# Kernel optimization log

Hardware: AMD Instinct MI355X
Metric: run time of the kernel (lower is better)

The kernel has to match this reference:

```python
import jax, jax.numpy as jnp
import numpy as np

NUM_HEADS = 12


def setup_inputs() -> dict:
    key = jax.random.key(0)
    ks = jax.random.split(key, 9)
    B, T, C = 4, 2048, 768
    s = 1.0 / np.sqrt(C)
    return {
        "x": jax.random.normal(ks[0], (B, T, C), dtype=jnp.float32),
        "wq": jax.random.normal(ks[1], (C, C), dtype=jnp.float32) * s,
        "bq": jnp.zeros((C,), dtype=jnp.float32),
        "wk": jax.random.normal(ks[2], (C, C), dtype=jnp.float32) * s,
        "bk": jnp.zeros((C,), dtype=jnp.float32),
        "wv": jax.random.normal(ks[3], (C, C), dtype=jnp.float32) * s,
        "bv": jnp.zeros((C,), dtype=jnp.float32),
        "wo": jax.random.normal(ks[4], (C, C), dtype=jnp.float32) * s,
        "bo": jnp.zeros((C,), dtype=jnp.float32),
    }


def reference(x, wq, bq, wk, bk, wv, bv, wo, bo):
    B, T, C = x.shape
    H = NUM_HEADS
    D = C // H
    scale = D ** -0.5
    # projections: weights stored as [in, out] so y = x @ w + b
    q = (x @ wq + bq).reshape(B, T, H, D).transpose(0, 2, 1, 3)  # [B,H,T,D]
    k = (x @ wk + bk).reshape(B, T, H, D).transpose(0, 2, 1, 3)
    v = (x @ wv + bv).reshape(B, T, H, D).transpose(0, 2, 1, 3)
    scores = jnp.einsum("bhqd,bhkd->bhqk", q, k) * scale  # [B,H,T,T]
    probs = jax.nn.softmax(scores, axis=-1)
    out = jnp.einsum("bhqk,bhkd->bhqd", probs, v)  # [B,H,T,D]
    out = out.transpose(0, 2, 1, 3).reshape(B, T, C)
    return out @ wo + bo
```

## Files before the change

kernel.cpp:

```cpp
#include <hip/hip_runtime.h>
#include <math.h>

#define NB 4
#define T_SEQ 2048
#define C_DIM 768
#define NH 12
#define HD 64
#define M_TOK (NB * T_SEQ)
#define NE ((size_t)M_TOK * C_DIM)
#define WE ((size_t)C_DIM * C_DIM)
#define QSCALE 0.18033688011112042f

typedef short bf16x8 __attribute__((ext_vector_type(8)));
typedef float f32x4 __attribute__((ext_vector_type(4)));
typedef unsigned short u16x4 __attribute__((ext_vector_type(4)));
typedef unsigned short u16x8 __attribute__((ext_vector_type(8)));
typedef unsigned short ushort_t;

__device__ __forceinline__ unsigned short f2bf(float x) {
    unsigned u = __float_as_uint(x);
    u += 0x7FFFu + ((u >> 16) & 1u);
    return (unsigned short)(u >> 16);
}
__device__ __forceinline__ float bf2f(unsigned short h) {
    return __uint_as_float(((unsigned)h) << 16);
}
__device__ __forceinline__ int sw128(int row, int bytecol) {
    return row * 128 + (bytecol ^ ((row & 7) << 4));
}
__device__ __forceinline__ void gload16(const ushort_t* gp, ushort_t* lp) {
    __builtin_amdgcn_global_load_lds(
        (const __attribute__((address_space(1))) unsigned int*)(const void*)gp,
        (__attribute__((address_space(3))) unsigned int*)(void*)lp, 16, 0, 0);
}

__global__ __launch_bounds__(256) void prep(
    const float* __restrict__ X,
    const float* __restrict__ wq, const float* __restrict__ wk,
    const float* __restrict__ wv, const float* __restrict__ wo,
    ushort_t* __restrict__ XH, ushort_t* __restrict__ Wbase)
{
    __shared__ float T[64][65];
    const int tid = threadIdx.x;
    const int bid = blockIdx.x;

    if (bid < 3072) {
        const size_t i = ((size_t)bid * 256 + tid) * 8;
        const float4 f0 = *(const float4*)&X[i];
        const float4 f1 = *(const float4*)&X[i + 4];
        const float xs[8] = {f0.x, f0.y, f0.z, f0.w, f1.x, f1.y, f1.z, f1.w};
        u16x8 h;
        #pragma unroll
        for (int j = 0; j < 8; ++j) h[j] = f2bf(xs[j]);
        *(u16x8*)&XH[i] = h;
        return;
    }

    const int r_ = bid - 3072;
    const int z = r_ / 144;
    const int rem = r_ % 144;
    const int ti = rem / 12, nj = rem % 12;
    const float* W = (z == 0) ? wq : (z == 1) ? wk : (z == 2) ? wv : wo;
    ushort_t* TH = Wbase + (size_t)z * 2 * WE;
    ushort_t* TL = TH + WE;
    {
        const int r = tid >> 2, cq = (tid & 3) * 16;
        #pragma unroll
        for (int j = 0; j < 4; ++j) {
            const float4 f = *(const float4*)&W[(size_t)(ti * 64 + r) * C_DIM + nj * 64 + cq + j * 4];
            T[r][cq + j * 4 + 0] = f.x;
            T[r][cq + j * 4 + 1] = f.y;
            T[r][cq + j * 4 + 2] = f.z;
            T[r][cq + j * 4 + 3] = f.w;
        }
    }
    __syncthreads();
    {
        const int n = tid >> 2, kq = (tid & 3) * 16;
        u16x8 h0, h1, l0, l1;
        #pragma unroll
        for (int j = 0; j < 8; ++j) {
            float v = T[kq + j][n];
            unsigned short hh = f2bf(v);
            h0[j] = hh; l0[j] = f2bf(v - bf2f(hh));
            v = T[kq + 8 + j][n];
            hh = f2bf(v);
            h1[j] = hh; l1[j] = f2bf(v - bf2f(hh));
        }
        const size_t o = (size_t)(nj * 64 + n) * C_DIM + ti * 64 + kq;
        *(u16x8*)&TH[o] = h0; *(u16x8*)&TH[o + 8] = h1;
        *(u16x8*)&TL[o] = l0; *(u16x8*)&TL[o + 8] = l1;
    }
}

__global__ __launch_bounds__(256, 4) void gemm_qkv(
    const ushort_t* __restrict__ XH,
    const ushort_t* __restrict__ WQH, const ushort_t* __restrict__ WKH,
    const ushort_t* __restrict__ WVH,
    const float* __restrict__ bq, const float* __restrict__ bk,
    const float* __restrict__ bv,
    ushort_t* __restrict__ Qo, ushort_t* __restrict__ Ko, ushort_t* __restrict__ VTo)
{
    __shared__ ushort_t TA[2][128 * 32];
    __shared__ ushort_t TB[2][128 * 32];

    const int tid = threadIdx.x, lane = tid & 63, w = tid >> 6;
    const int l15 = lane & 15, g = lane >> 4;
    const int wr = w >> 1, wc = w & 1;

    int bid = (int)blockIdx.x;
    bid = (bid & 7) * 144 + (bid >> 3);
    const int bm = bid / 18, bn = bid % 18;
    const int wsel = bn / 6, bnw = bn % 6;

    const ushort_t* BH = (wsel == 0) ? WQH : (wsel == 1) ? WKH : WVH;
    const float* bias = (wsel == 0) ? bq : (wsel == 1) ? bk : bv;

    f32x4 acc[4][4];
    #pragma unroll
    for (int m = 0; m < 4; ++m)
        #pragma unroll
        for (int n = 0; n < 4; ++n) acc[m][n] = (f32x4){0.f, 0.f, 0.f, 0.f};

    auto stage = [&](int buf, int k0) {
        #pragma unroll
        for (int p = 0; p < 4; ++p) {
            const int cb = 256 * p + 64 * w;
            const int c  = cb + lane;
            const int row = (c & 511) >> 2;
            const int slot = (c & 3) ^ ((row >> 1) & 3);
            if (cb < 512)
                gload16(XH + ((size_t)bm * 128 + row) * C_DIM + k0 + slot * 8,
                        &TA[buf][(cb & 511) * 8]);
            else
                gload16(BH + ((size_t)bnw * 128 + row) * C_DIM + k0 + slot * 8,
                        &TB[buf][(cb & 511) * 8]);
        }
    };

    stage(0, 0);
    int cur = 0;
    if (wsel < 2) {
        for (int k0 = 0; k0 < C_DIM; k0 += 32) {
            __syncthreads();
            if (k0 + 32 < C_DIM) stage(cur ^ 1, k0 + 32);
            bf16x8 ah[4], bh_[4];
            #pragma unroll
            for (int m = 0; m < 4; ++m) {
                const int r = 64 * wr + 16 * m + l15;
                const int off = r * 64 + ((g ^ ((r >> 1) & 3)) << 4);
                ah[m] = *(const bf16x8*)((const char*)TA[cur] + off);
            }
            #pragma unroll
            for (int n = 0; n < 4; ++n) {
                const int r = 64 * wc + 16 * n + l15;
                const int off = r * 64 + ((g ^ ((r >> 1) & 3)) << 4);
                bh_[n] = *(const bf16x8*)((const char*)TB[cur] + off);
            }
            #pragma unroll
            for (int m = 0; m < 4; ++m)
                #pragma unroll
                for (int n = 0; n < 4; ++n)
                    acc[m][n] = __builtin_amdgcn_mfma_f32_16x16x32_bf16(bh_[n], ah[m], acc[m][n], 0, 0, 0);
            cur ^= 1;
        }
        const float oscale = (wsel == 0) ? QSCALE : 1.0f;
        ushort_t* OH = (wsel == 0) ? Qo : Ko;
        #pragma unroll
        for (int n = 0; n < 4; ++n) {
            const int colw0 = bnw * 128 + 64 * wc + 16 * n + 4 * g;
            const float4 bv4 = *(const float4*)&bias[colw0];
            const float bvr[4] = {bv4.x, bv4.y, bv4.z, bv4.w};
            const int h = colw0 >> 6, d0 = colw0 & 63;
            #pragma unroll
            for (int m = 0; m < 4; ++m) {
                const int t = bm * 128 + 64 * wr + 16 * m + l15;
                const int b = t >> 11, tt = t & (T_SEQ - 1);
                u16x4 ph;
                #pragma unroll
                for (int r = 0; r < 4; ++r)
                    ph[r] = f2bf((acc[m][n][r] + bvr[r]) * oscale);
                *(u16x4*)&OH[(((size_t)b * NH + h) * T_SEQ + tt) * HD + d0] = ph;
            }
        }
    } else {
        for (int k0 = 0; k0 < C_DIM; k0 += 32) {
            __syncthreads();
            if (k0 + 32 < C_DIM) stage(cur ^ 1, k0 + 32);
            bf16x8 ah[4], bh_[4];
            #pragma unroll
            for (int m = 0; m < 4; ++m) {
                const int r = 64 * wr + 16 * m + l15;
                const int off = r * 64 + ((g ^ ((r >> 1) & 3)) << 4);
                ah[m] = *(const bf16x8*)((const char*)TA[cur] + off);
            }
            #pragma unroll
            for (int n = 0; n < 4; ++n) {
                const int r = 64 * wc + 16 * n + l15;
                const int off = r * 64 + ((g ^ ((r >> 1) & 3)) << 4);
                bh_[n] = *(const bf16x8*)((const char*)TB[cur] + off);
            }
            #pragma unroll
            for (int m = 0; m < 4; ++m)
                #pragma unroll
                for (int n = 0; n < 4; ++n)
                    acc[m][n] = __builtin_amdgcn_mfma_f32_16x16x32_bf16(ah[m], bh_[n], acc[m][n], 0, 0, 0);
            cur ^= 1;
        }
        #pragma unroll
        for (int n = 0; n < 4; ++n) {
            const int colw = bnw * 128 + 64 * wc + 16 * n + l15;
            const float bv_ = bias[colw];
            const int h = colw >> 6, d = colw & 63;
            #pragma unroll
            for (int m = 0; m < 4; ++m) {
                const int row0 = bm * 128 + 64 * wr + 16 * m + 4 * g;
                u16x4 ph;
                #pragma unroll
                for (int r = 0; r < 4; ++r) ph[r] = f2bf(acc[m][n][r] + bv_);
                const int b = row0 >> 11, t0 = row0 & (T_SEQ - 1);
                *(u16x4*)&VTo[(((size_t)b * NH + h) * HD + d) * T_SEQ + t0] = ph;
            }
        }
    }
}

__global__ __launch_bounds__(256, 4) void gemm_out(
    const ushort_t* __restrict__ AB,
    const ushort_t* __restrict__ BH, const ushort_t* __restrict__ BL,
    const float* __restrict__ bias, float* __restrict__ OutF)
{
    __shared__ ushort_t TA[2][128 * 32];
    __shared__ ushort_t TB[2][2][64 * 32];

    const int tid = threadIdx.x, lane = tid & 63, w = tid >> 6;
    const int l15 = lane & 15, g = lane >> 4;
    const int wr = w >> 1, wc = w & 1;

    int bid = (int)blockIdx.x;
    bid = (bid & 7) * 96 + (bid >> 3);
    const int bm = bid / 12, bn = bid % 12;

    f32x4 acc[4][2];
    #pragma unroll
    for (int m = 0; m < 4; ++m)
        #pragma unroll
        for (int n = 0; n < 2; ++n) acc[m][n] = (f32x4){0.f, 0.f, 0.f, 0.f};

    auto stage = [&](int buf, int k0) {
        #pragma unroll
        for (int p = 0; p < 4; ++p) {
            const int c = w + 4 * p;
            if (c < 8) {
                const int row = c * 16 + (lane >> 2);
                const int slot = (lane & 3) ^ ((row >> 1) & 3);
                gload16(AB + ((size_t)bm * 128 + row) * C_DIM + k0 + slot * 8,
                        &TA[buf][c * 512]);
            } else {
                const int t_ = (c - 8) >> 2;
                const int cc = c & 3;
                const int row = cc * 16 + (lane >> 2);
                const int slot = (lane & 3) ^ ((row >> 1) & 3);
                const ushort_t* src = (t_ ? BL : BH) + ((size_t)bn * 64 + row) * C_DIM + k0 + slot * 8;
                gload16(src, &TB[buf][t_][cc * 512]);
            }
        }
    };

    stage(0, 0);
    int cur = 0;
    for (int k0 = 0; k0 < C_DIM; k0 += 32) {
        __syncthreads();
        if (k0 + 32 < C_DIM) stage(cur ^ 1, k0 + 32);

        bf16x8 a_[4], bh_[2], bl_[2];
        #pragma unroll
        for (int m = 0; m < 4; ++m) {
            const int r = 64 * wr + 16 * m + l15;
            const int off = r * 64 + ((g ^ ((r >> 1) & 3)) << 4);
            a_[m] = *(const bf16x8*)((const char*)TA[cur] + off);
        }
        #pragma unroll
        for (int n = 0; n < 2; ++n) {
            const int r = 32 * wc + 16 * n + l15;
            const int off = r * 64 + ((g ^ ((r >> 1) & 3)) << 4);
            bh_[n] = *(const bf16x8*)((const char*)TB[cur][0] + off);
            bl_[n] = *(const bf16x8*)((const char*)TB[cur][1] + off);
        }
        #pragma unroll
        for (int m = 0; m < 4; ++m)
            #pragma unroll
            for (int n = 0; n < 2; ++n) {
                acc[m][n] = __builtin_amdgcn_mfma_f32_16x16x32_bf16(a_[m], bh_[n], acc[m][n], 0, 0, 0);
                acc[m][n] = __builtin_amdgcn_mfma_f32_16x16x32_bf16(a_[m], bl_[n], acc[m][n], 0, 0, 0);
            }
        cur ^= 1;
    }

    #pragma unroll
    for (int n = 0; n < 2; ++n) {
        const int col = bn * 64 + 32 * wc + 16 * n + l15;
        const float bv = bias[col];
        #pragma unroll
        for (int m = 0; m < 4; ++m) {
            const int row0 = bm * 128 + 64 * wr + 16 * m + 4 * g;
            #pragma unroll
            for (int r = 0; r < 4; ++r)
                OutF[(size_t)(row0 + r) * C_DIM + col] = acc[m][n][r] + bv;
        }
    }
}

__global__ __launch_bounds__(256, 3) void attn_fuse9(
    const ushort_t* __restrict__ QB, const ushort_t* __restrict__ KB,
    const ushort_t* __restrict__ VTB, ushort_t* __restrict__ ABo)
{
    __shared__ ushort_t Ks[2][64 * 64];
    __shared__ ushort_t Vt[2][64 * 64];
    __shared__ ushort_t Pm[4][32 * 64];

    const int tid = threadIdx.x, lane = tid & 63, w = tid >> 6;
    const int l15 = lane & 15, g = lane >> 4;

    int bid = (int)blockIdx.x;
    bid = (bid & 7) * 96 + (bid >> 3);
    const int bh = bid >> 4, qt = bid & 15;
    const int b = bh / NH, h = bh % NH;

    bf16x8 qf0[2], qf1[2];
    #pragma unroll
    for (int kc = 0; kc < 2; ++kc) {
        const size_t base = ((size_t)bh * T_SEQ + qt * 128 + 32 * w + l15) * HD + kc * 32 + g * 8;
        qf0[kc] = *(const bf16x8*)&QB[base];
        qf1[kc] = *(const bf16x8*)&QB[base + (size_t)16 * HD];
    }

    bf16x8 onesf;
    #pragma unroll
    for (int j = 0; j < 8; ++j) onesf[j] = (short)0x3F80;

    f32x4 o0[4], o1[4];
    #pragma unroll
    for (int nd = 0; nd < 4; ++nd) {
        o0[nd] = (f32x4){0.f, 0.f, 0.f, 0.f};
        o1[nd] = (f32x4){0.f, 0.f, 0.f, 0.f};
    }
    f32x4 ol0 = (f32x4){0.f, 0.f, 0.f, 0.f};
    f32x4 ol1 = (f32x4){0.f, 0.f, 0.f, 0.f};

    const ushort_t* kb = KB + (size_t)bh * T_SEQ * HD;
    const ushort_t* vb = VTB + (size_t)bh * HD * T_SEQ;
    const int swz = (l15 & 7) << 4;

    const ushort_t *gK0, *gK1, *gV0, *gV1;
    {
        const int c0 = w * 64 + lane;
        const int r0 = c0 >> 3;
        const int cb0 = ((c0 & 7) * 16) ^ ((r0 & 7) << 4);
        gK0 = kb + (size_t)r0 * HD + (cb0 >> 1);
        gV0 = vb + (size_t)r0 * T_SEQ + (cb0 >> 1);
        const int c1 = c0 + 256;
        const int r1 = c1 >> 3;
        const int cb1 = ((c1 & 7) * 16) ^ ((r1 & 7) << 4);
        gK1 = kb + (size_t)r1 * HD + (cb1 >> 1);
        gV1 = vb + (size_t)r1 * T_SEQ + (cb1 >> 1);
    }
    ushort_t* dK0 = &Ks[0][w * 512];
    ushort_t* dK1 = &Ks[0][2048 + w * 512];
    ushort_t* dV0 = &Vt[0][w * 512];
    ushort_t* dV1 = &Vt[0][2048 + w * 512];

    for (int kt = 0; kt < T_SEQ; kt += 128) {
        __syncthreads();
        gload16(gK0, dK0);
        gload16(gK1, dK1);
        gload16(gV0, dV0);
        gload16(gV1, dV1);
        gload16(gK0 + (size_t)64 * HD, dK0 + 4096);
        gload16(gK1 + (size_t)64 * HD, dK1 + 4096);
        gload16(gV0 + 64, dV0 + 4096);
        gload16(gV1 + 64, dV1 + 4096);
        gK0 += (size_t)128 * HD; gK1 += (size_t)128 * HD;
        gV0 += 128; gV1 += 128;
        __syncthreads();

        #pragma unroll
        for (int half = 0; half < 2; ++half) {
            const char* ksb = (const char*)Ks[half];
            const char* vtb = (const char*)Vt[half];

            f32x4 s0[4], s1[4];
            #pragma unroll
            for (int nb = 0; nb < 4; ++nb) {
                s0[nb] = (f32x4){0.f, 0.f, 0.f, 0.f};
                s1[nb] = (f32x4){0.f, 0.f, 0.f, 0.f};
            }
            __builtin_amdgcn_s_setprio(1);
            #pragma unroll
            for (int kc = 0; kc < 2; ++kc)
                #pragma unroll
                for (int nb = 0; nb < 4; ++nb) {
                    const bf16x8 kf = *(const bf16x8*)(ksb + sw128(16 * nb + l15, kc * 64 + g * 16));
                    s0[nb] = __builtin_amdgcn_mfma_f32_16x16x32_bf16(kf, qf0[kc], s0[nb], 0, 0, 0);
                    s1[nb] = __builtin_amdgcn_mfma_f32_16x16x32_bf16(kf, qf1[kc], s1[nb], 0, 0, 0);
                }
            __builtin_amdgcn_s_setprio(0);

            #pragma unroll
            for (int nb = 0; nb < 4; ++nb) {
                const float a0 = __builtin_amdgcn_exp2f(s0[nb][0]);
                const float a1 = __builtin_amdgcn_exp2f(s0[nb][1]);
                const float a2 = __builtin_amdgcn_exp2f(s0[nb][2]);
                const float a3 = __builtin_amdgcn_exp2f(s0[nb][3]);
                const unsigned dwa0 = __builtin_amdgcn_perm(
                    __float_as_uint(a1), __float_as_uint(a0), 0x07060302u);
                const unsigned dwa1 = __builtin_amdgcn_perm(
                    __float_as_uint(a3), __float_as_uint(a2), 0x07060302u);
                *(uint2*)((char*)Pm[w] + l15 * 128 + ((32 * nb + 8 * g) ^ swz)) =
                    make_uint2(dwa0, dwa1);

                const float b0 = __builtin_amdgcn_exp2f(s1[nb][0]);
                const float b1 = __builtin_amdgcn_exp2f(s1[nb][1]);
                const float b2 = __builtin_amdgcn_exp2f(s1[nb][2]);
                const float b3 = __builtin_amdgcn_exp2f(s1[nb][3]);
                const unsigned dwb0 = __builtin_amdgcn_perm(
                    __float_as_uint(b1), __float_as_uint(b0), 0x07060302u);
                const unsigned dwb1 = __builtin_amdgcn_perm(
                    __float_as_uint(b3), __float_as_uint(b2), 0x07060302u);
                *(uint2*)((char*)Pm[w] + (16 + l15) * 128 + ((32 * nb + 8 * g) ^ swz)) =
                    make_uint2(dwb0, dwb1);
            }

            __builtin_amdgcn_s_setprio(1);
            #pragma unroll
            for (int kc2 = 0; kc2 < 2; ++kc2) {
                const bf16x8 pb0 = *(const bf16x8*)((const char*)Pm[w] + l15 * 128 + ((kc2 * 64 + g * 16) ^ swz));
                const bf16x8 pb1 = *(const bf16x8*)((const char*)Pm[w] + (16 + l15) * 128 + ((kc2 * 64 + g * 16) ^ swz));
                #pragma unroll
                for (int nd = 0; nd < 4; ++nd) {
                    const bf16x8 vf = *(const bf16x8*)(vtb + sw128(16 * nd + l15, kc2 * 64 + g * 16));
                    o0[nd] = __builtin_amdgcn_mfma_f32_16x16x32_bf16(vf, pb0, o0[nd], 0, 0, 0);
                    o1[nd] = __builtin_amdgcn_mfma_f32_16x16x32_bf16(vf, pb1, o1[nd], 0, 0, 0);
                }
                ol0 = __builtin_amdgcn_mfma_f32_16x16x32_bf16(onesf, pb0, ol0, 0, 0, 0);
                ol1 = __builtin_amdgcn_mfma_f32_16x16x32_bf16(onesf, pb1, ol1, 0, 0, 0);
            }
            __builtin_amdgcn_s_setprio(0);
        }
    }

    const float inv0 = 1.0f / ol0[0];
    const float inv1 = 1.0f / ol1[0];
    const int t0 = qt * 128 + 32 * w + l15;
    #pragma unroll
    for (int nd = 0; nd < 4; ++nd) {
        u16x4 h0_, h1_;
        #pragma unroll
        for (int r = 0; r < 4; ++r) {
            h0_[r] = f2bf(o0[nd][r] * inv0);
            h1_[r] = f2bf(o1[nd][r] * inv1);
        }
        const size_t col = h * HD + 16 * nd + 4 * g;
        *(u16x4*)&ABo[((size_t)b * T_SEQ + t0) * C_DIM + col] = h0_;
        *(u16x4*)&ABo[((size_t)b * T_SEQ + t0 + 16) * C_DIM + col] = h1_;
    }
}

extern "C" void kernel_launch(void* const* d_in, const int* in_sizes, int n_in,
                              void* d_out, int out_size, void* d_ws, size_t ws_size,
                              hipStream_t stream)
{
    const float* x  = (const float*)d_in[0];
    const float* wq = (const float*)d_in[1];
    const float* bq = (const float*)d_in[2];
    const float* wk = (const float*)d_in[3];
    const float* bk = (const float*)d_in[4];
    const float* wv = (const float*)d_in[5];
    const float* bv = (const float*)d_in[6];
    const float* wo = (const float*)d_in[7];
    const float* bo = (const float*)d_in[8];

    ushort_t* Wbase = (ushort_t*)d_ws;
    ushort_t* WQ_H = Wbase;
    ushort_t* WK_H = Wbase + 2 * WE;
    ushort_t* WV_H = Wbase + 4 * WE;
    ushort_t* WO_H = Wbase + 6 * WE;
    ushort_t* WO_L = WO_H + WE;
    ushort_t* X_H  = Wbase + 8 * WE;
    ushort_t* K_B  = X_H + 2 * NE;
    ushort_t* VT_B = K_B + NE;
    ushort_t* Q_B = (ushort_t*)d_out;
    ushort_t* A_B = X_H;

    const dim3 blk(256);

    prep<<<3648, blk, 0, stream>>>(x, wq, wk, wv, wo, X_H, Wbase);

    gemm_qkv<<<1152, blk, 0, stream>>>(X_H, WQ_H, WK_H, WV_H,
                                       bq, bk, bv, Q_B, K_B, VT_B);

    attn_fuse9<<<768, blk, 0, stream>>>(Q_B, K_B, VT_B, A_B);

    gemm_out<<<768, blk, 0, stream>>>(A_B, WO_H, WO_L, bo, (float*)d_out);
}
```

Measured before the change: 147.2 us.

## Switch attention to 32x32x16 MFMA and keep P in registers via permlane swap

Rewrites the attention kernel to use 32x32x16 bf16 MFMA tiles instead of 16x16x32. The exponentiated score accumulator is repacked directly into the B-operand layout with permlane32_swap, so the per-wave LDS staging buffer for P and its stores and loads go away. The prep kernel also writes the low-part weight split only for the output projection weight, skipping unused stores for Q/K/V. This raises accumulator register pressure (three f32x16 accumulators plus the score tiles), which may affect occupancy at the three-blocks-per-SM bound.

```diff
diff --git a/kernel.cpp b/kernel.cpp
--- a/kernel.cpp
+++ b/kernel.cpp
@@ -13,6 +13,8 @@
 
 typedef short bf16x8 __attribute__((ext_vector_type(8)));
 typedef float f32x4 __attribute__((ext_vector_type(4)));
+typedef float f32x16 __attribute__((ext_vector_type(16)));
+typedef unsigned u32x2 __attribute__((ext_vector_type(2)));
 typedef unsigned short u16x4 __attribute__((ext_vector_type(4)));
 typedef unsigned short u16x8 __attribute__((ext_vector_type(8)));
 typedef unsigned short ushort_t;
@@ -32,6 +34,9 @@
     __builtin_amdgcn_global_load_lds(
         (const __attribute__((address_space(1))) unsigned int*)(const void*)gp,
         (__attribute__((address_space(3))) unsigned int*)(void*)lp, 16, 0, 0);
+}
+__device__ __forceinline__ unsigned pkbf(float hi, float lo) {
+    return __builtin_amdgcn_perm(__float_as_uint(hi), __float_as_uint(lo), 0x07060302u);
 }
 
 __global__ __launch_bounds__(256) void prep(
@@ -89,7 +94,9 @@
         }
         const size_t o = (size_t)(nj * 64 + n) * C_DIM + ti * 64 + kq;
         *(u16x8*)&TH[o] = h0; *(u16x8*)&TH[o + 8] = h1;
-        *(u16x8*)&TL[o] = l0; *(u16x8*)&TL[o + 8] = l1;
+        if (z == 3) {
+            *(u16x8*)&TL[o] = l0; *(u16x8*)&TL[o + 8] = l1;
+        }
     }
 }
 
@@ -311,46 +318,35 @@
     }
 }
 
-__global__ __launch_bounds__(256, 3) void attn_fuse9(
+__global__ __launch_bounds__(256, 3) void attn_fuse11(
     const ushort_t* __restrict__ QB, const ushort_t* __restrict__ KB,
     const ushort_t* __restrict__ VTB, ushort_t* __restrict__ ABo)
 {
     __shared__ ushort_t Ks[2][64 * 64];
     __shared__ ushort_t Vt[2][64 * 64];
-    __shared__ ushort_t Pm[4][32 * 64];
 
     const int tid = threadIdx.x, lane = tid & 63, w = tid >> 6;
-    const int l15 = lane & 15, g = lane >> 4;
+    const int l31 = lane & 31, hl = lane >> 5;
 
     int bid = (int)blockIdx.x;
     bid = (bid & 7) * 96 + (bid >> 3);
     const int bh = bid >> 4, qt = bid & 15;
-    const int b = bh / NH, h = bh % NH;
-
-    bf16x8 qf0[2], qf1[2];
-    #pragma unroll
-    for (int kc = 0; kc < 2; ++kc) {
-        const size_t base = ((size_t)bh * T_SEQ + qt * 128 + 32 * w + l15) * HD + kc * 32 + g * 8;
-        qf0[kc] = *(const bf16x8*)&QB[base];
-        qf1[kc] = *(const bf16x8*)&QB[base + (size_t)16 * HD];
-    }
+    const int b = bh / NH, hed = bh % NH;
+
+    bf16x8 qf[4];
+    const size_t qrow = (size_t)bh * T_SEQ + qt * 128 + 32 * w + l31;
+    #pragma unroll
+    for (int ks = 0; ks < 4; ++ks)
+        qf[ks] = *(const bf16x8*)&QB[qrow * HD + ks * 16 + 8 * hl];
 
     bf16x8 onesf;
     #pragma unroll
     for (int j = 0; j < 8; ++j) onesf[j] = (short)0x3F80;
 
-    f32x4 o0[4], o1[4];
-    #pragma unroll
-    for (int nd = 0; nd < 4; ++nd) {
-        o0[nd] = (f32x4){0.f, 0.f, 0.f, 0.f};
-        o1[nd] = (f32x4){0.f, 0.f, 0.f, 0.f};
-    }
-    f32x4 ol0 = (f32x4){0.f, 0.f, 0.f, 0.f};
-    f32x4 ol1 = (f32x4){0.f, 0.f, 0.f, 0.f};
+    f32x16 oA = (f32x16)(0.f), oB = (f32x16)(0.f), ol = (f32x16)(0.f);
 
     const ushort_t* kb = KB + (size_t)bh * T_SEQ * HD;
     const ushort_t* vb = VTB + (size_t)bh * HD * T_SEQ;
-    const int swz = (l15 & 7) << 4;
 
     const ushort_t *gK0, *gK1, *gV0, *gV1;
     {
@@ -369,6 +365,22 @@
     ushort_t* dK1 = &Ks[0][2048 + w * 512];
     ushort_t* dV0 = &Vt[0][w * 512];
     ushort_t* dV1 = &Vt[0][2048 + w * 512];
+
+    auto mkfrag = [&](const f32x16& s, int base) -> bf16x8 {
+        const unsigned D0 = pkbf(__builtin_amdgcn_exp2f(s[base + 1]),
+                                 __builtin_amdgcn_exp2f(s[base + 0]));
+        const unsigned D1 = pkbf(__builtin_amdgcn_exp2f(s[base + 3]),
+                                 __builtin_amdgcn_exp2f(s[base + 2]));
+        const unsigned D2 = pkbf(__builtin_amdgcn_exp2f(s[base + 5]),
+                                 __builtin_amdgcn_exp2f(s[base + 4]));
+        const unsigned D3 = pkbf(__builtin_amdgcn_exp2f(s[base + 7]),
+                                 __builtin_amdgcn_exp2f(s[base + 6]));
+        const u32x2 r02 = __builtin_amdgcn_permlane32_swap(D0, D2, false, false);
+        const u32x2 r13 = __builtin_amdgcn_permlane32_swap(D1, D3, false, false);
+        union { unsigned u[4]; bf16x8 v; } cv;
+        cv.u[0] = r02[0]; cv.u[1] = r13[0]; cv.u[2] = r02[1]; cv.u[3] = r13[1];
+        return cv.v;
+    };
 
     for (int kt = 0; kt < T_SEQ; kt += 128) {
         __syncthreads();
@@ -389,80 +401,52 @@
             const char* ksb = (const char*)Ks[half];
             const char* vtb = (const char*)Vt[half];
 
-            f32x4 s0[4], s1[4];
-            #pragma unroll
-            for (int nb = 0; nb < 4; ++nb) {
-                s0[nb] = (f32x4){0.f, 0.f, 0.f, 0.f};
-                s1[nb] = (f32x4){0.f, 0.f, 0.f, 0.f};
-            }
+            f32x16 sA = (f32x16)(0.f), sB = (f32x16)(0.f);
             __builtin_amdgcn_s_setprio(1);
             #pragma unroll
-            for (int kc = 0; kc < 2; ++kc)
-                #pragma unroll
-                for (int nb = 0; nb < 4; ++nb) {
-                    const bf16x8 kf = *(const bf16x8*)(ksb + sw128(16 * nb + l15, kc * 64 + g * 16));
-                    s0[nb] = __builtin_amdgcn_mfma_f32_16x16x32_bf16(kf, qf0[kc], s0[nb], 0, 0, 0);
-                    s1[nb] = __builtin_amdgcn_mfma_f32_16x16x32_bf16(kf, qf1[kc], s1[nb], 0, 0, 0);
-                }
+            for (int ks = 0; ks < 4; ++ks) {
+                const int bc = ks * 32 + 16 * hl;
+                const bf16x8 kfA = *(const bf16x8*)(ksb + sw128(l31, bc));
+                const bf16x8 kfB = *(const bf16x8*)(ksb + sw128(32 + l31, bc));
+                sA = __builtin_amdgcn_mfma_f32_32x32x16_bf16(kfA, qf[ks], sA, 0, 0, 0);
+                sB = __builtin_amdgcn_mfma_f32_32x32x16_bf16(kfB, qf[ks], sB, 0, 0, 0);
+            }
             __builtin_amdgcn_s_setprio(0);
 
-            #pragma unroll
-            for (int nb = 0; nb < 4; ++nb) {
-                const float a0 = __builtin_amdgcn_exp2f(s0[nb][0]);
-                const float a1 = __builtin_amdgcn_exp2f(s0[nb][1]);
-                const float a2 = __builtin_amdgcn_exp2f(s0[nb][2]);
-                const float a3 = __builtin_amdgcn_exp2f(s0[nb][3]);
-                const unsigned dwa0 = __builtin_amdgcn_perm(
-                    __float_as_uint(a1), __float_as_uint(a0), 0x07060302u);
-                const unsigned dwa1 = __builtin_amdgcn_perm(
-                    __float_as_uint(a3), __float_as_uint(a2), 0x07060302u);
-                *(uint2*)((char*)Pm[w] + l15 * 128 + ((32 * nb + 8 * g) ^ swz)) =
-                    make_uint2(dwa0, dwa1);
-
-                const float b0 = __builtin_amdgcn_exp2f(s1[nb][0]);
-                const float b1 = __builtin_amdgcn_exp2f(s1[nb][1]);
-                const float b2 = __builtin_amdgcn_exp2f(s1[nb][2]);
-                const float b3 = __builtin_amdgcn_exp2f(s1[nb][3]);
-                const unsigned dwb0 = __builtin_amdgcn_perm(
-                    __float_as_uint(b1), __float_as_uint(b0), 0x07060302u);
-                const unsigned dwb1 = __builtin_amdgcn_perm(
-                    __float_as_uint(b3), __float_as_uint(b2), 0x07060302u);
-                *(uint2*)((char*)Pm[w] + (16 + l15) * 128 + ((32 * nb + 8 * g) ^ swz)) =
-                    make_uint2(dwb0, dwb1);
-            }
+            bf16x8 pb0 = mkfrag(sA, 0);
+            bf16x8 pb1 = mkfrag(sA, 8);
+            bf16x8 pb2 = mkfrag(sB, 0);
+            bf16x8 pb3 = mkfrag(sB, 8);
 
             __builtin_amdgcn_s_setprio(1);
             #pragma unroll
-            for (int kc2 = 0; kc2 < 2; ++kc2) {
-                const bf16x8 pb0 = *(const bf16x8*)((const char*)Pm[w] + l15 * 128 + ((kc2 * 64 + g * 16) ^ swz));
-                const bf16x8 pb1 = *(const bf16x8*)((const char*)Pm[w] + (16 + l15) * 128 + ((kc2 * 64 + g * 16) ^ swz));
-                #pragma unroll
-                for (int nd = 0; nd < 4; ++nd) {
-                    const bf16x8 vf = *(const bf16x8*)(vtb + sw128(16 * nd + l15, kc2 * 64 + g * 16));
-                    o0[nd] = __builtin_amdgcn_mfma_f32_16x16x32_bf16(vf, pb0, o0[nd], 0, 0, 0);
-                    o1[nd] = __builtin_amdgcn_mfma_f32_16x16x32_bf16(vf, pb1, o1[nd], 0, 0, 0);
-                }
-                ol0 = __builtin_amdgcn_mfma_f32_16x16x32_bf16(onesf, pb0, ol0, 0, 0, 0);
-                ol1 = __builtin_amdgcn_mfma_f32_16x16x32_bf16(onesf, pb1, ol1, 0, 0, 0);
+            for (int ki = 0; ki < 4; ++ki) {
+                const bf16x8 pb = (ki == 0) ? pb0 : (ki == 1) ? pb1 : (ki == 2) ? pb2 : pb3;
+                const int bc = ki * 32 + 16 * hl;
+                const bf16x8 vfA = *(const bf16x8*)(vtb + sw128(l31, bc));
+                const bf16x8 vfB = *(const bf16x8*)(vtb + sw128(32 + l31, bc));
+                oA = __builtin_amdgcn_mfma_f32_32x32x16_bf16(vfA, pb, oA, 0, 0, 0);
+                oB = __builtin_amdgcn_mfma_f32_32x32x16_bf16(vfB, pb, oB, 0, 0, 0);
+                ol = __builtin_amdgcn_mfma_f32_32x32x16_bf16(onesf, pb, ol, 0, 0, 0);
             }
             __builtin_amdgcn_s_setprio(0);
         }
     }
 
-    const float inv0 = 1.0f / ol0[0];
-    const float inv1 = 1.0f / ol1[0];
-    const int t0 = qt * 128 + 32 * w + l15;
-    #pragma unroll
-    for (int nd = 0; nd < 4; ++nd) {
-        u16x4 h0_, h1_;
+    const float inv = 1.0f / ol[0];
+    const int t = qt * 128 + 32 * w + l31;
+    const size_t obase = ((size_t)b * T_SEQ + t) * C_DIM + hed * HD;
+    #pragma unroll
+    for (int b2 = 0; b2 < 4; ++b2) {
+        u16x4 ha, hb;
         #pragma unroll
         for (int r = 0; r < 4; ++r) {
-            h0_[r] = f2bf(o0[nd][r] * inv0);
-            h1_[r] = f2bf(o1[nd][r] * inv1);
-        }
-        const size_t col = h * HD + 16 * nd + 4 * g;
-        *(u16x4*)&ABo[((size_t)b * T_SEQ + t0) * C_DIM + col] = h0_;
-        *(u16x4*)&ABo[((size_t)b * T_SEQ + t0 + 16) * C_DIM + col] = h1_;
+            ha[r] = f2bf(oA[4 * b2 + r] * inv);
+            hb[r] = f2bf(oB[4 * b2 + r] * inv);
+        }
+        const int d0 = 8 * b2 + 4 * hl;
+        *(u16x4*)&ABo[obase + d0] = ha;
+        *(u16x4*)&ABo[obase + 32 + d0] = hb;
     }
 }
 
@@ -499,7 +483,7 @@
     gemm_qkv<<<1152, blk, 0, stream>>>(X_H, WQ_H, WK_H, WV_H,
                                        bq, bk, bv, Q_B, K_B, VT_B);
 
-    attn_fuse9<<<768, blk, 0, stream>>>(Q_B, K_B, VT_B, A_B);
+    attn_fuse11<<<768, blk, 0, stream>>>(Q_B, K_B, VT_B, A_B);
 
     gemm_out<<<768, blk, 0, stream>>>(A_B, WO_H, WO_L, bo, (float*)d_out);
 }
```

Result: slower. 150.1 us (+2.0%).
